# Kernel tuning notes

Measured on AMD Instinct MI355X. Metric: run time of the kernel, lower is better.

The kernel has to match this reference:

```python
import jax, jax.numpy as jnp
import numpy as np

N, E, IN_DIM, HID, NUM_CLASSES = 100000, 1600000, 256, 128, 40


def setup_inputs() -> dict:
    key = jax.random.key(0)
    ks = jax.random.split(key, 16)
    f32 = jnp.float32

    def w(k, shape):
        fan_in = shape[0]
        return (jax.random.normal(k, shape, f32) / jnp.sqrt(jnp.asarray(fan_in, f32)))

    x = jax.random.normal(ks[0], (N, IN_DIM), f32)
    edge_index = jax.random.randint(ks[1], (2, E), 0, N, dtype=jnp.int32)
    adj_embed = jax.random.normal(ks[2], (N, HID), f32) * 0.02  # xavier-ish
    return {
        "x": x,
        "edge_index": edge_index,
        "adj_embed": adj_embed,
        "wx1": w(ks[3], (IN_DIM, HID)), "bx1": jnp.zeros((HID,), f32),
        "wx2": w(ks[4], (HID, HID)),    "bx2": jnp.zeros((HID,), f32),
        "wa1": w(ks[5], (HID, HID)),    "ba1": jnp.zeros((HID,), f32),
        "wa2": w(ks[6], (HID, HID)),    "ba2": jnp.zeros((HID,), f32),
        "ww1": w(ks[7], (2 * HID, HID)), "bw1": jnp.zeros((HID,), f32),
        "wc": w(ks[8], (HID, NUM_CLASSES)), "bc": jnp.zeros((NUM_CLASSES,), f32),
    }


def _aggregate_neighbours(edge_index, weights, num_nodes):
    src, dst = edge_index[0], edge_index[1]
    # scatter-sum of gathered rows [E, HID] into [num_nodes, HID]
    agg = jax.ops.segment_sum(weights[src], dst, num_segments=num_nodes)
    deg = jax.ops.segment_sum(jnp.ones_like(dst, dtype=weights.dtype), dst,
                              num_segments=num_nodes)
    deg = jnp.maximum(deg, 1.0)[:, None]
    return agg / deg


def reference(x, edge_index, adj_embed, wx1, bx1, wx2, bx2,
              wa1, ba1, wa2, ba2, ww1, bw1, wc, bc):
    # mlp_x (dropout = identity in eval mode)
    hx = jax.nn.relu(x @ wx1 + bx1) @ wx2 + bx2          # [N, HID]
    # adjacency branch: mean-aggregate learned node embeddings over edges
    ha_raw = _aggregate_neighbours(edge_index, adj_embed, adj_embed.shape[0])
    ha = jax.nn.relu(ha_raw @ wa1 + ba1) @ wa2 + ba2     # [N, HID]
    # mlp_w over concat (num_layers=1 -> single Linear+ReLU)
    combined = jnp.concatenate([hx, ha], axis=1)         # [N, 2*HID]
    h = jax.nn.relu(combined @ ww1 + bw1)                # [N, HID]
    h = jax.nn.relu(h + hx + ha)
    logits = h @ wc + bc                                 # [N, NUM_CLASSES]
    return logits
```

## Files before the change

kernel.cpp:

```cpp
#include <hip/hip_runtime.h>

#define Nn 100000
#define Ee 1600000
#define IND 256
#define HD 128
#define NCLS 40
#define NBLK 391

typedef _Float16 f16;
typedef f16 f16x8 __attribute__((ext_vector_type(8)));
typedef f16 f16x4 __attribute__((ext_vector_type(4)));
typedef float f32x4 __attribute__((ext_vector_type(4)));

extern "C" __global__ void __launch_bounds__(256)
k_hist(const int* __restrict__ ei, int* __restrict__ counts) {
    int e = blockIdx.x * 256 + threadIdx.x;
    if (e < Ee) atomicAdd(&counts[ei[Ee + e]], 1);
}

extern "C" __global__ void __launch_bounds__(256)
k_scan1(const int* __restrict__ counts, int* __restrict__ bsum) {
    __shared__ int s[256];
    int t = threadIdx.x;
    int i = blockIdx.x * 256 + t;
    s[t] = (i < Nn) ? counts[i] : 0;
    __syncthreads();
    for (int d = 128; d > 0; d >>= 1) {
        if (t < d) s[t] += s[t + d];
        __syncthreads();
    }
    if (t == 0) bsum[blockIdx.x] = s[0];
}

extern "C" __global__ void __launch_bounds__(512)
k_scan2(int* __restrict__ bsum) {
    __shared__ int s[512];
    int t = threadIdx.x;
    int v = (t < NBLK) ? bsum[t] : 0;
    s[t] = v;
    __syncthreads();
    for (int d = 1; d < 512; d <<= 1) {
        int x = (t >= d) ? s[t - d] : 0;
        __syncthreads();
        s[t] += x;
        __syncthreads();
    }
    if (t < NBLK) bsum[t] = s[t] - v;
}

extern "C" __global__ void __launch_bounds__(256)
k_scan3(const int* __restrict__ counts, const int* __restrict__ bsum,
        int* __restrict__ offsets) {
    __shared__ int s[256];
    int t = threadIdx.x;
    int i = blockIdx.x * 256 + t;
    int v = (i < Nn) ? counts[i] : 0;
    s[t] = v;
    __syncthreads();
    for (int d = 1; d < 256; d <<= 1) {
        int x = (t >= d) ? s[t - d] : 0;
        __syncthreads();
        s[t] += x;
        __syncthreads();
    }
    if (i < Nn) offsets[i] = bsum[blockIdx.x] + s[t] - v;
    if (i == 0) offsets[Nn] = Ee;
}

extern "C" __global__ void __launch_bounds__(256)
k_scatter(const int* __restrict__ ei, const int* __restrict__ offsets,
          int* __restrict__ counts, int* __restrict__ bucket) {
    int e = blockIdx.x * 256 + threadIdx.x;
    if (e >= Ee) return;
    int dst = ei[Ee + e];
    int r = atomicSub(&counts[dst], 1);
    bucket[offsets[dst] + r - 1] = ei[e];
}

extern "C" __global__ void __launch_bounds__(256)
k_prep(const float* __restrict__ wx1, const float* __restrict__ wx2,
       const float* __restrict__ wa1, const float* __restrict__ wa2,
       const float* __restrict__ ww1, const float* __restrict__ wc,
       f16* __restrict__ wp,
       const float* __restrict__ emb, f16* __restrict__ embh) {
    int idx = blockIdx.x * 256 + threadIdx.x;
    if (idx >= 120832) {
        int i = idx - 120832;
        const float4* p = (const float4*)emb + (size_t)i * 2;
        float4 a = p[0], b = p[1];
        f16x8 h;
        h[0] = (f16)a.x; h[1] = (f16)a.y; h[2] = (f16)a.z; h[3] = (f16)a.w;
        h[4] = (f16)b.x; h[5] = (f16)b.y; h[6] = (f16)b.z; h[7] = (f16)b.w;
        *(f16x8*)(embh + (size_t)i * 8) = h;
        return;
    }
    const float* W;
    int K, base;
    if (idx < 32768)       { W = wx1; K = 256; base = 0; }
    else if (idx < 49152)  { W = wx2; K = 128; base = 32768; }
    else if (idx < 65536)  { W = wa1; K = 128; base = 49152; }
    else if (idx < 81920)  { W = wa2; K = 128; base = 65536; }
    else if (idx < 114688) { W = ww1; K = 256; base = 81920; }
    else {
        int local = idx - 114688;
        int j = local & 7;
        int L = (local >> 3) & 63;
        int kt = (local >> 9) & 3;
        int ft = local / 2048;
        int k = kt * 32 + (L >> 4) * 8 + j;
        int n = ft * 16 + (L & 15);
        wp[idx] = (n < NCLS) ? (f16)wc[k * NCLS + n] : (f16)0.f;
        return;
    }
    int local = idx - base;
    int KT = K >> 5;
    int j = local & 7;
    int L = (local >> 3) & 63;
    int kt = (local >> 9) % KT;
    int ft = local / (512 * KT);
    int k = kt * 32 + (L >> 4) * 8 + j;
    int n = ft * 16 + (L & 15);
    wp[idx] = (f16)W[k * HD + n];
}

extern "C" __global__ void __launch_bounds__(256)
k_gather(const int* __restrict__ offsets, const int* __restrict__ bucket,
         const f16* __restrict__ embh, f16* __restrict__ harawp) {
    int t = threadIdx.x;
    int lane = t & 63;
    int node = blockIdx.x * 4 + (t >> 6);
    int q = lane >> 4;
    int cl = (lane & 15) * 8;

    int beg = offsets[node];
    int end = offsets[node + 1];
    int deg = end - beg;

    int myidx = (lane < deg) ? bucket[beg + lane] : 0;

    float s[8];
#pragma unroll
    for (int j = 0; j < 8; j++) s[j] = 0.f;

    int dlim = (deg < 64) ? deg : 64;
    int e = q;
    for (; e + 4 < dlim; e += 8) {
        int a0 = __shfl(myidx, e);
        int a1 = __shfl(myidx, e + 4);
        f16x8 v0 = *(const f16x8*)(embh + (size_t)a0 * HD + cl);
        f16x8 v1 = *(const f16x8*)(embh + (size_t)a1 * HD + cl);
#pragma unroll
        for (int j = 0; j < 8; j++) s[j] += (float)v0[j] + (float)v1[j];
    }
    if (e < dlim) {
        int a0 = __shfl(myidx, e);
        f16x8 v0 = *(const f16x8*)(embh + (size_t)a0 * HD + cl);
#pragma unroll
        for (int j = 0; j < 8; j++) s[j] += (float)v0[j];
    }
    for (int i = beg + 64 + q; i < end; i += 4) {
        int a0 = bucket[i];
        f16x8 v0 = *(const f16x8*)(embh + (size_t)a0 * HD + cl);
#pragma unroll
        for (int j = 0; j < 8; j++) s[j] += (float)v0[j];
    }

#pragma unroll
    for (int j = 0; j < 8; j++) {
        s[j] += __shfl_down(s[j], 32);
        s[j] += __shfl_down(s[j], 16);
    }

    if (lane < 16) {
        float inv = 1.0f / fmaxf((float)deg, 1.0f);
        f16x8 h;
#pragma unroll
        for (int j = 0; j < 8; j++) h[j] = (f16)(s[j] * inv);
        int nt = node >> 4, m = node & 15;
        int kt = lane >> 2, q2 = lane & 3;
        *(f16x8*)(harawp + (((nt * 4 + kt) * 64 + m + 16 * q2) * 8)) = h;
    }
}

extern "C" __global__ void __launch_bounds__(256, 4)
linkx_mlp(const float* __restrict__ x, const f16* __restrict__ harawp,
          const f16* __restrict__ wx1p, const float* __restrict__ bx1,
          const f16* __restrict__ wx2p, const float* __restrict__ bx2,
          const f16* __restrict__ wa1p, const float* __restrict__ ba1,
          const f16* __restrict__ wa2p, const float* __restrict__ ba2,
          const f16* __restrict__ ww1p, const float* __restrict__ bw1,
          const f16* __restrict__ wcp, const float* __restrict__ bc,
          float* __restrict__ out) {
    __shared__ __align__(16) f16 shr[4096];
    __shared__ __align__(16) f16 hxp[4096];
    __shared__ __align__(16) f16 hap[4096];

    const int t = threadIdx.x;
    const int node0 = blockIdx.x * 32;
    const int lane = t & 63;
    const int wid = t >> 6;
    const int mt = wid >> 1;
    const int fh = wid & 1;

    f32x4 acc[4];
    float rreg[4][4];

#define INIT_ACC(BIAS)                                                    \
    _Pragma("unroll")                                                     \
    for (int q = 0; q < 4; q++) {                                         \
        float bv = (BIAS)[(fh * 4 + q) * 16 + (lane & 15)];               \
        acc[q][0] = bv; acc[q][1] = bv; acc[q][2] = bv; acc[q][3] = bv;   \
    }

#define GEMM_K128(APACK, BP)                                                  \
    _Pragma("unroll")                                                         \
    for (int kt = 0; kt < 4; kt++) {                                          \
        f16x8 a = *(const f16x8*)((APACK) + ((mt * 4 + kt) * 64 + lane) * 8); \
        _Pragma("unroll")                                                     \
        for (int q = 0; q < 4; q++) {                                         \
            f16x8 b = *(const f16x8*)((BP) + (((fh*4+q)*4 + kt)*64 + lane)*8);\
            acc[q] = __builtin_amdgcn_mfma_f32_16x16x32_f16(a, b, acc[q], 0, 0, 0); \
        }                                                                     \
    }

#define EPILOGUE(MODE, PDST)                                                  \
    _Pragma("unroll")                                                         \
    for (int q = 0; q < 4; q++) {                                             \
        int f = (fh * 4 + q) * 16 + (lane & 15);                              \
        int kt2 = f >> 5, q2 = (f >> 3) & 3, j2 = f & 7;                      \
        _Pragma("unroll")                                                     \
        for (int r = 0; r < 4; r++) {                                         \
            int n = (lane >> 4) * 4 + r;                                      \
            float v = acc[q][r];                                              \
            if (MODE == 0) v = fmaxf(v, 0.f);                                 \
            if (MODE == 1) rreg[q][r] = v;                                    \
            if (MODE == 2) rreg[q][r] += v;                                   \
            if (MODE == 3) v = fmaxf(fmaxf(v, 0.f) + rreg[q][r], 0.f);        \
            (PDST)[((mt * 4 + kt2) * 64 + n + 16 * q2) * 8 + j2] = (f16)v;    \
        }                                                                     \
    }

    INIT_ACC(bx1)
    {
        const float* xbase = x + (size_t)(node0 + mt * 16 + (lane & 15)) * IND
                               + (lane >> 4) * 8;
        float4 u[16];
#pragma unroll
        for (int kt = 0; kt < 8; kt++) {
            u[2 * kt]     = *(const float4*)(xbase + kt * 32);
            u[2 * kt + 1] = *(const float4*)(xbase + kt * 32 + 4);
        }
#pragma unroll
        for (int kt = 0; kt < 8; kt++) {
            float4 u0 = u[2 * kt], u1 = u[2 * kt + 1];
            f16x8 a;
            a[0] = (f16)u0.x; a[1] = (f16)u0.y; a[2] = (f16)u0.z; a[3] = (f16)u0.w;
            a[4] = (f16)u1.x; a[5] = (f16)u1.y; a[6] = (f16)u1.z; a[7] = (f16)u1.w;
#pragma unroll
            for (int q = 0; q < 4; q++) {
                f16x8 b = *(const f16x8*)(wx1p + (((fh*4+q)*8 + kt)*64 + lane)*8);
                acc[q] = __builtin_amdgcn_mfma_f32_16x16x32_f16(a, b, acc[q], 0, 0, 0);
            }
        }
    }
    EPILOGUE(0, shr)
    __syncthreads();

    INIT_ACC(bx2)
    GEMM_K128(shr, wx2p)
    EPILOGUE(1, hxp)
    __syncthreads();

    INIT_ACC(ba1)
    {
        int ntb = (node0 >> 4) + mt;
        f16x8 av[4];
#pragma unroll
        for (int kt = 0; kt < 4; kt++)
            av[kt] = *(const f16x8*)(harawp + ((ntb * 4 + kt) * 64 + lane) * 8);
#pragma unroll
        for (int kt = 0; kt < 4; kt++) {
#pragma unroll
            for (int q = 0; q < 4; q++) {
                f16x8 b = *(const f16x8*)(wa1p + (((fh*4+q)*4 + kt)*64 + lane)*8);
                acc[q] = __builtin_amdgcn_mfma_f32_16x16x32_f16(av[kt], b, acc[q], 0, 0, 0);
            }
        }
    }
    EPILOGUE(0, shr)
    __syncthreads();

    INIT_ACC(ba2)
    GEMM_K128(shr, wa2p)
    EPILOGUE(2, hap)
    __syncthreads();

    INIT_ACC(bw1)
#pragma unroll
    for (int kt = 0; kt < 8; kt++) {
        const f16* ap = (kt < 4) ? (hxp + ((mt * 4 + kt) * 64 + lane) * 8)
                                 : (hap + ((mt * 4 + (kt - 4)) * 64 + lane) * 8);
        f16x8 a = *(const f16x8*)ap;
#pragma unroll
        for (int q = 0; q < 4; q++) {
            f16x8 b = *(const f16x8*)(ww1p + (((fh*4+q)*8 + kt)*64 + lane)*8);
            acc[q] = __builtin_amdgcn_mfma_f32_16x16x32_f16(a, b, acc[q], 0, 0, 0);
        }
    }
    EPILOGUE(3, shr)
    __syncthreads();

    {
        int nft = (fh == 0) ? 2 : 1;
#pragma unroll 2
        for (int ii = 0; ii < nft; ii++) {
            int ft = (ii == 0) ? fh : 2;
            int f = ft * 16 + (lane & 15);
            f32x4 c;
            float bv = (f < NCLS) ? bc[f] : 0.f;
            c[0] = bv; c[1] = bv; c[2] = bv; c[3] = bv;
#pragma unroll
            for (int kt = 0; kt < 4; kt++) {
                f16x8 a = *(const f16x8*)(shr + ((mt * 4 + kt) * 64 + lane) * 8);
                f16x8 b = *(const f16x8*)(wcp + ((ft * 4 + kt) * 64 + lane) * 8);
                c = __builtin_amdgcn_mfma_f32_16x16x32_f16(a, b, c, 0, 0, 0);
            }
            if (f < NCLS) {
#pragma unroll
                for (int r = 0; r < 4; r++) {
                    int n = node0 + mt * 16 + (lane >> 4) * 4 + r;
                    out[(size_t)n * NCLS + f] = c[r];
                }
            }
        }
    }
}

extern "C" void kernel_launch(void* const* d_in, const int* in_sizes, int n_in,
                              void* d_out, int out_size, void* d_ws, size_t ws_size,
                              hipStream_t stream) {
    const float* x   = (const float*)d_in[0];
    const int*   ei  = (const int*)d_in[1];
    const float* emb = (const float*)d_in[2];
    const float* wx1 = (const float*)d_in[3];
    const float* bx1 = (const float*)d_in[4];
    const float* wx2 = (const float*)d_in[5];
    const float* bx2 = (const float*)d_in[6];
    const float* wa1 = (const float*)d_in[7];
    const float* ba1 = (const float*)d_in[8];
    const float* wa2 = (const float*)d_in[9];
    const float* ba2 = (const float*)d_in[10];
    const float* ww1 = (const float*)d_in[11];
    const float* bw1 = (const float*)d_in[12];
    const float* wc  = (const float*)d_in[13];
    const float* bc  = (const float*)d_in[14];
    float* out = (float*)d_out;

    int* ws = (int*)d_ws;
    int* counts  = ws;
    int* offsets = ws + 2 * Nn;
    int* bsum    = ws + 3 * Nn + 16;
    int* bucket  = ws + 3 * Nn + 512;
    f16* wp      = (f16*)(ws + 3 * Nn + 512 + Ee);
    f16* wx1p = wp;
    f16* wx2p = wp + 32768;
    f16* wa1p = wp + 49152;
    f16* wa2p = wp + 65536;
    f16* ww1p = wp + 81920;
    f16* wcp  = wp + 114688;
    f16* harawp = wp + 131072;
    f16* embh   = harawp + (size_t)Nn * HD;

    hipMemsetAsync(ws, 0, (size_t)Nn * sizeof(int), stream);

    k_prep<<<6722, 256, 0, stream>>>(wx1, wx2, wa1, wa2, ww1, wc, wp, emb, embh);
    k_hist<<<Ee / 256, 256, 0, stream>>>(ei, counts);
    k_scan1<<<NBLK, 256, 0, stream>>>(counts, bsum);
    k_scan2<<<1, 512, 0, stream>>>(bsum);
    k_scan3<<<NBLK, 256, 0, stream>>>(counts, bsum, offsets);
    k_scatter<<<Ee / 256, 256, 0, stream>>>(ei, offsets, counts, bucket);
    k_gather<<<Nn / 4, 256, 0, stream>>>(offsets, bucket, embh, harawp);

    linkx_mlp<<<Nn / 32, 256, 0, stream>>>(x, harawp,
                                           wx1p, bx1, wx2p, bx2,
                                           wa1p, ba1, wa2p, ba2,
                                           ww1p, bw1, wcp, bc, out);
}
```

Before: 492.1 us.

## Fuse histogram into prep kernel, record edge ranks, drop scan2 and atomic scatter

Interleaves the degree histogram with the weight/embedding prep blocks in one launch, and stores each edge's atomicAdd return value as its rank. The scatter then places edges without a second atomic pass. The single-block scan2 is removed: each scan3 block sums the preceding block totals itself. This cuts two kernel launches and one round of atomics, at the cost of writing and reading a rank array that reuses the harawp buffer, plus redundant prefix work in scan3.

```diff
diff --git a/kernel.cpp b/kernel.cpp
--- a/kernel.cpp
+++ b/kernel.cpp
@@ -13,81 +13,31 @@
 typedef float f32x4 __attribute__((ext_vector_type(4)));
 
 extern "C" __global__ void __launch_bounds__(256)
-k_hist(const int* __restrict__ ei, int* __restrict__ counts) {
-    int e = blockIdx.x * 256 + threadIdx.x;
-    if (e < Ee) atomicAdd(&counts[ei[Ee + e]], 1);
-}
-
-extern "C" __global__ void __launch_bounds__(256)
-k_scan1(const int* __restrict__ counts, int* __restrict__ bsum) {
-    __shared__ int s[256];
-    int t = threadIdx.x;
-    int i = blockIdx.x * 256 + t;
-    s[t] = (i < Nn) ? counts[i] : 0;
-    __syncthreads();
-    for (int d = 128; d > 0; d >>= 1) {
-        if (t < d) s[t] += s[t + d];
-        __syncthreads();
-    }
-    if (t == 0) bsum[blockIdx.x] = s[0];
-}
-
-extern "C" __global__ void __launch_bounds__(512)
-k_scan2(int* __restrict__ bsum) {
-    __shared__ int s[512];
-    int t = threadIdx.x;
-    int v = (t < NBLK) ? bsum[t] : 0;
-    s[t] = v;
-    __syncthreads();
-    for (int d = 1; d < 512; d <<= 1) {
-        int x = (t >= d) ? s[t - d] : 0;
-        __syncthreads();
-        s[t] += x;
-        __syncthreads();
-    }
-    if (t < NBLK) bsum[t] = s[t] - v;
-}
-
-extern "C" __global__ void __launch_bounds__(256)
-k_scan3(const int* __restrict__ counts, const int* __restrict__ bsum,
-        int* __restrict__ offsets) {
-    __shared__ int s[256];
-    int t = threadIdx.x;
-    int i = blockIdx.x * 256 + t;
-    int v = (i < Nn) ? counts[i] : 0;
-    s[t] = v;
-    __syncthreads();
-    for (int d = 1; d < 256; d <<= 1) {
-        int x = (t >= d) ? s[t - d] : 0;
-        __syncthreads();
-        s[t] += x;
-        __syncthreads();
-    }
-    if (i < Nn) offsets[i] = bsum[blockIdx.x] + s[t] - v;
-    if (i == 0) offsets[Nn] = Ee;
-}
-
-extern "C" __global__ void __launch_bounds__(256)
-k_scatter(const int* __restrict__ ei, const int* __restrict__ offsets,
-          int* __restrict__ counts, int* __restrict__ bucket) {
-    int e = blockIdx.x * 256 + threadIdx.x;
-    if (e >= Ee) return;
-    int dst = ei[Ee + e];
-    int r = atomicSub(&counts[dst], 1);
-    bucket[offsets[dst] + r - 1] = ei[e];
-}
-
-extern "C" __global__ void __launch_bounds__(256)
 k_prep(const float* __restrict__ wx1, const float* __restrict__ wx2,
        const float* __restrict__ wa1, const float* __restrict__ wa2,
        const float* __restrict__ ww1, const float* __restrict__ wc,
        f16* __restrict__ wp,
-       const float* __restrict__ emb, f16* __restrict__ embh) {
-    int idx = blockIdx.x * 256 + threadIdx.x;
+       const float* __restrict__ emb, f16* __restrict__ embh,
+       const int* __restrict__ ei, int* __restrict__ counts,
+       int* __restrict__ rank) {
+    int bid = blockIdx.x;
+    int p;
+    if (bid < 12500) {
+        if (bid & 1) {
+            int e = (bid >> 1) * 256 + threadIdx.x;
+            int dst = ei[Ee + e];
+            rank[e] = atomicAdd(&counts[dst], 1);
+            return;
+        }
+        p = bid >> 1;
+    } else {
+        p = 6250 + (bid - 12500);
+    }
+    int idx = p * 256 + threadIdx.x;
     if (idx >= 120832) {
         int i = idx - 120832;
-        const float4* p = (const float4*)emb + (size_t)i * 2;
-        float4 a = p[0], b = p[1];
+        const float4* pp = (const float4*)emb + (size_t)i * 2;
+        float4 a = pp[0], b = pp[1];
         f16x8 h;
         h[0] = (f16)a.x; h[1] = (f16)a.y; h[2] = (f16)a.z; h[3] = (f16)a.w;
         h[4] = (f16)b.x; h[5] = (f16)b.y; h[6] = (f16)b.z; h[7] = (f16)b.w;
@@ -121,6 +71,58 @@
     int k = kt * 32 + (L >> 4) * 8 + j;
     int n = ft * 16 + (L & 15);
     wp[idx] = (f16)W[k * HD + n];
+}
+
+extern "C" __global__ void __launch_bounds__(256)
+k_scan1(const int* __restrict__ counts, int* __restrict__ bsum) {
+    __shared__ int s[256];
+    int t = threadIdx.x;
+    int i = blockIdx.x * 256 + t;
+    s[t] = (i < Nn) ? counts[i] : 0;
+    __syncthreads();
+    for (int d = 128; d > 0; d >>= 1) {
+        if (t < d) s[t] += s[t + d];
+        __syncthreads();
+    }
+    if (t == 0) bsum[blockIdx.x] = s[0];
+}
+
+extern "C" __global__ void __launch_bounds__(256)
+k_scan3(const int* __restrict__ counts, const int* __restrict__ bsum,
+        int* __restrict__ offsets) {
+    __shared__ int s[256];
+    __shared__ int basev;
+    int t = threadIdx.x;
+    int i = blockIdx.x * 256 + t;
+    int partial = 0;
+    for (int k = t; k < blockIdx.x; k += 256) partial += bsum[k];
+    s[t] = partial;
+    __syncthreads();
+    for (int d = 128; d > 0; d >>= 1) {
+        if (t < d) s[t] += s[t + d];
+        __syncthreads();
+    }
+    if (t == 0) basev = s[0];
+    __syncthreads();
+    int v = (i < Nn) ? counts[i] : 0;
+    s[t] = v;
+    __syncthreads();
+    for (int d = 1; d < 256; d <<= 1) {
+        int x = (t >= d) ? s[t - d] : 0;
+        __syncthreads();
+        s[t] += x;
+        __syncthreads();
+    }
+    if (i < Nn) offsets[i] = basev + s[t] - v;
+    if (i == 0) offsets[Nn] = Ee;
+}
+
+extern "C" __global__ void __launch_bounds__(256)
+k_scatter2(const int* __restrict__ ei, const int* __restrict__ offsets,
+           const int* __restrict__ rank, int* __restrict__ bucket) {
+    int e = blockIdx.x * 256 + threadIdx.x;
+    int dst = ei[Ee + e];
+    bucket[offsets[dst] + rank[e]] = ei[e];
 }
 
 extern "C" __global__ void __launch_bounds__(256)
@@ -370,15 +372,15 @@
     f16* wcp  = wp + 114688;
     f16* harawp = wp + 131072;
     f16* embh   = harawp + (size_t)Nn * HD;
+    int* rank = (int*)harawp;
 
     hipMemsetAsync(ws, 0, (size_t)Nn * sizeof(int), stream);
 
-    k_prep<<<6722, 256, 0, stream>>>(wx1, wx2, wa1, wa2, ww1, wc, wp, emb, embh);
-    k_hist<<<Ee / 256, 256, 0, stream>>>(ei, counts);
+    k_prep<<<12972, 256, 0, stream>>>(wx1, wx2, wa1, wa2, ww1, wc, wp,
+                                      emb, embh, ei, counts, rank);
     k_scan1<<<NBLK, 256, 0, stream>>>(counts, bsum);
-    k_scan2<<<1, 512, 0, stream>>>(bsum);
     k_scan3<<<NBLK, 256, 0, stream>>>(counts, bsum, offsets);
-    k_scatter<<<Ee / 256, 256, 0, stream>>>(ei, offsets, counts, bucket);
+    k_scatter2<<<Ee / 256, 256, 0, stream>>>(ei, offsets, rank, bucket);
     k_gather<<<Nn / 4, 256, 0, stream>>>(offsets, bucket, embh, harawp);
 
     linkx_mlp<<<Nn / 32, 256, 0, stream>>>(x, harawp,
```

New measurement: 428.4 us. -12.9%, faster.
